# Performance work log

Hardware: AMD Instinct MI355X
Metric: run time of the kernel (lower is better)

The kernel has to match this reference:

```python
import jax, jax.numpy as jnp
import numpy as np
from jax import lax

B, C_IN, H, W = 16, 256, 64, 64
C_OUT, K_SZ, N_EXP, RED_C = 256, 3, 4, 16  # reduction_channels = max(256//16,16)=16


def setup_inputs() -> dict:
    key = jax.random.key(0)
    ks = jax.random.split(key, 6)
    x = jax.random.normal(ks[0], (B, C_IN, H, W), dtype=jnp.float32)
    # routing network params (1x1 convs == dense on pooled features)
    w1 = jax.random.normal(ks[1], (RED_C, C_IN), dtype=jnp.float32) * (1.0 / np.sqrt(C_IN))
    b1 = jnp.zeros((RED_C,), dtype=jnp.float32)
    w2 = jax.random.normal(ks[2], (N_EXP * C_IN, RED_C), dtype=jnp.float32) * (1.0 / np.sqrt(RED_C))
    b2 = jnp.zeros((N_EXP * C_IN,), dtype=jnp.float32)
    # expert weight bank (num_experts, c_out, c_in, kh, kw)
    fan_in = C_IN * K_SZ * K_SZ
    bound = np.sqrt(6.0 / fan_in)  # kaiming_uniform with a=sqrt(5) ~ U(-sqrt(6/fan_in)*..., simplified scale)
    weight = jax.random.uniform(ks[3], (N_EXP, C_OUT, C_IN, K_SZ, K_SZ), dtype=jnp.float32, minval=-bound, maxval=bound)
    return {"x": x, "w1": w1, "b1": b1, "w2": w2, "b2": b2, "weight": weight}


def reference(x, w1, b1, w2, b2, weight):
    b = x.shape[0]
    # route_func: global avg pool -> 1x1 conv -> relu -> 1x1 conv -> sigmoid
    pooled = jnp.mean(x, axis=(2, 3))                       # (b, c_in)
    r = jax.nn.relu(pooled @ w1.T + b1)                     # (b, red_c)
    rw = jax.nn.sigmoid(r @ w2.T + b2)                      # (b, K*c_in)
    rw = rw.reshape(b, N_EXP, C_IN)                         # (b, K, c_in)
    # per-sample combined kernel: sum over experts, routing scales input channels
    combined = jnp.einsum('bkc,kocij->bocij', rw, weight)   # (b, c_out, c_in, kh, kw)
    # per-sample conv (equivalent to groups=b trick in torch)
    def conv_one(xi, wi):
        return lax.conv_general_dilated(
            xi[None], wi, window_strides=(1, 1), padding=[(1, 1), (1, 1)],
            dimension_numbers=('NCHW', 'OIHW', 'NCHW'))[0]
    out = jax.vmap(conv_one)(x, combined)                   # (b, c_out, h, w)
    return out
```

## Files before the change

kernel.cpp:

```cpp
#include <hip/hip_runtime.h>
#include <hip/hip_bf16.h>
#include <math.h>

#define BB   16
#define CIN  256
#define HH   64
#define WW   64
#define COUT 256
#define NEXP 4
#define REDC 16
#define HW   (HH*WW)

typedef __attribute__((ext_vector_type(8))) short short8;
typedef __attribute__((ext_vector_type(16))) float f32x16;

#define AS1 __attribute__((address_space(1)))
#define AS3 __attribute__((address_space(3)))

__device__ __forceinline__ void gld_lds16(void* lds, const void* gp) {
    __builtin_amdgcn_global_load_lds((const AS1 unsigned int*)gp,
                                     (AS3 unsigned int*)lds, 16, 0, 0);
}

__global__ __launch_bounds__(256)
void transpose_pool_kernel(const float* __restrict__ x, ushort* __restrict__ xT,
                           float* __restrict__ pp) {
    int blk = blockIdx.x;
    int sq = blk & 3;
    int chunk = (blk >> 2) & 7;
    int b = blk >> 5;
    int c0 = chunk * 32;
    int s0 = sq * 1024;
    int tid = threadIdx.x;
    const float* xb = x + ((size_t)(b * CIN + c0)) * HW;

    float psum[32];
    #pragma unroll
    for (int i = 0; i < 32; ++i) psum[i] = 0.f;

    for (int it = 0; it < 4; ++it) {
        int s = s0 + it * 256 + tid;
        unsigned int pk[16];
        #pragma unroll
        for (int p = 0; p < 16; ++p) {
            float lo = xb[(size_t)(2 * p) * HW + s];
            float hi = xb[(size_t)(2 * p + 1) * HW + s];
            psum[2 * p]     += lo;
            psum[2 * p + 1] += hi;
            asm volatile("v_cvt_pk_bf16_f32 %0, %1, %2" : "=v"(pk[p]) : "v"(lo), "v"(hi));
        }
        #pragma unroll
        for (int q = 0; q < 4; ++q) {
            ushort* dst = xT + ((size_t)(b * 32 + chunk * 4 + q) * HW + s) * 8;
            *(uint4*)dst = make_uint4(pk[q * 4], pk[q * 4 + 1], pk[q * 4 + 2], pk[q * 4 + 3]);
        }
    }

    __shared__ float red[4][32];
    int lane = tid & 63, wid = tid >> 6;
    #pragma unroll
    for (int i = 0; i < 32; ++i) {
        float v = psum[i];
        #pragma unroll
        for (int off = 32; off > 0; off >>= 1) v += __shfl_down(v, off, 64);
        if (lane == 0) red[wid][i] = v;
    }
    __syncthreads();
    if (tid < 32)
        pp[(b * 4 + sq) * 256 + c0 + tid] = red[0][tid] + red[1][tid] + red[2][tid] + red[3][tid];
}

__global__ void route_kernel(const float* __restrict__ pp,
                             const float* __restrict__ w1, const float* __restrict__ b1,
                             const float* __restrict__ w2, const float* __restrict__ b2,
                             float* __restrict__ rw) {
    __shared__ float p_s[BB][CIN];
    __shared__ float r_s[BB][REDC];
    int tid = threadIdx.x;
    for (int i = tid; i < BB * CIN; i += 256) {
        int b = i >> 8, c = i & 255;
        p_s[b][c] = (pp[(b * 4 + 0) * 256 + c] + pp[(b * 4 + 1) * 256 + c] +
                     pp[(b * 4 + 2) * 256 + c] + pp[(b * 4 + 3) * 256 + c]) * (1.0f / HW);
    }
    __syncthreads();
    {
        int b = tid >> 4, j = tid & 15;
        float acc = b1[j];
        for (int c = 0; c < CIN; ++c) acc += p_s[b][c] * w1[j * CIN + c];
        r_s[b][j] = fmaxf(acc, 0.f);
    }
    __syncthreads();
    for (int i = tid; i < BB * NEXP * CIN; i += 256) {
        int b = i >> 10, o2 = i & 1023;
        float acc = b2[o2];
        #pragma unroll
        for (int j = 0; j < REDC; ++j) acc += r_s[b][j] * w2[o2 * REDC + j];
        rw[i] = 1.f / (1.f + expf(-acc));
    }
}

__global__ __launch_bounds__(256)
void combine3_kernel(const float* __restrict__ rw,
                     const float* __restrict__ weight,
                     ushort* __restrict__ cw) {
    int blk = blockIdx.x;
    int u = blk >> 1;
    int t = (blk & 1) * 256 + threadIdx.x;
    int gg = u & 1;
    int v = u >> 1;
    int t9 = v % 9;
    int cu = v / 9;
    int chunk16 = cu & 15;
    int ot = cu >> 4;
    int o_loc = t >> 3, c8 = t & 7;
    int o = ot * 64 + o_loc;
    int c = chunk16 * 16 + gg * 8 + c8;

    __shared__ float rw_s[16][4][8];
    int tid = threadIdx.x;
    #pragma unroll
    for (int r = 0; r < 2; ++r) {
        int i = r * 256 + tid;
        if (i < 512) {
            int b = i >> 5, k = (i >> 3) & 3, cc = i & 7;
            rw_s[b][k][cc] = rw[b * 1024 + k * 256 + chunk16 * 16 + gg * 8 + cc];
        }
    }
    __syncthreads();

    float wk0 = weight[((size_t)(0 * COUT + o) * CIN + c) * 9 + t9];
    float wk1 = weight[((size_t)(1 * COUT + o) * CIN + c) * 9 + t9];
    float wk2 = weight[((size_t)(2 * COUT + o) * CIN + c) * 9 + t9];
    float wk3 = weight[((size_t)(3 * COUT + o) * CIN + c) * 9 + t9];

    size_t base = (size_t)u * 512 + t;
    #pragma unroll
    for (int b = 0; b < 16; ++b) {
        float acc = rw_s[b][0][c8] * wk0 + rw_s[b][1][c8] * wk1 +
                    rw_s[b][2][c8] * wk2 + rw_s[b][3][c8] * wk3;
        __hip_bfloat16 hv = __float2bfloat16(acc);
        cw[base + (size_t)b * 589824] = *(ushort*)&hv;
    }
}

__global__ __launch_bounds__(512, 2)
void conv_mfma(const ushort* __restrict__ xT, const ushort* __restrict__ cw,
               float* __restrict__ out, const ushort* __restrict__ zp) {
    __shared__ char LDS[2][57472];

    int blk = blockIdx.x;
    int L = (blk & 7) * 32 + (blk >> 3);
    int b  = L >> 4;
    int rt = (L >> 2) & 3;
    int ot = L & 3;
    int r0 = rt * 16, o0 = ot * 64;
    int tid = threadIdx.x;
    int lane = tid & 63, wid = tid >> 6;
    int l31 = lane & 31, h = lane >> 5;

    f32x16 acc[2][4];
    #pragma unroll
    for (int mi = 0; mi < 2; ++mi)
        #pragma unroll
        for (int f = 0; f < 4; ++f) acc[mi][f] = (f32x16)0.f;

    const char* xTb = (const char*)(xT + (size_t)b * 32 * HW * 8);
    const ushort* Ab = cw + (size_t)((b * 4 + ot) * 16) * 9216;

    const char* srcb[7];
    int dsto[7];
    int strd[7];
    #pragma unroll
    for (int i = 0; i < 7; ++i) {
        int u = wid * 7 + i;
        if (u < 18) {
            srcb[i] = (const char*)(Ab + (size_t)u * 512) + lane * 16;
            dsto[i] = u * 1024;
            strd[i] = 18432;
        } else if (u < 54) {
            int ux = u - 18;
            int r = ux >> 1, half = ux & 1;
            int grow = r0 - 1 + r;
            bool valid = (grow >= 0 && grow < 64);
            srcb[i] = valid
                ? xTb + (size_t)(half * HW + grow * 64) * 16 + lane * 16
                : (const char*)zp + lane * 16;
            dsto[i] = 18432 + (half * 1188 + r * 66 + 1) * 16;
            strd[i] = valid ? 131072 : 0;
        } else {
            srcb[i] = (const char*)zp + lane * 16;
            dsto[i] = 56448;
            strd[i] = 0;
        }
    }

    char* ldsb = &LDS[0][0];

    for (int i = tid; i < 28736; i += 512) ((unsigned int*)ldsb)[i] = 0;
    __syncthreads();

    #define STAGE(BUF, CH)                                                    \
    {                                                                         \
        _Pragma("unroll")                                                     \
        for (int i = 0; i < 7; ++i)                                           \
            gld_lds16(ldsb + (BUF) * 57472 + dsto[i],                         \
                      srcb[i] + (size_t)(CH) * strd[i]);                      \
    }

    #define LOADT(T, va0, va1, vb0, vb1, vb2, vb3)                            \
    {                                                                         \
        const int di_ = (T) / 3, dj_ = (T) - di_ * 3;                         \
        va0 = *(const short8*)&asb[(((T) * 2 + h) * 64 + 0  + l31) * 8];      \
        va1 = *(const short8*)&asb[(((T) * 2 + h) * 64 + 32 + l31) * 8];      \
        const int rr_ = wid * 2 + di_;                                        \
        vb0 = *(const short8*)&xsb[(rr_ * 66 +  0 + l31 + dj_) * 8];          \
        vb1 = *(const short8*)&xsb[(rr_ * 66 + 32 + l31 + dj_) * 8];          \
        vb2 = *(const short8*)&xsb[((rr_ + 1) * 66 +  0 + l31 + dj_) * 8];    \
        vb3 = *(const short8*)&xsb[((rr_ + 1) * 66 + 32 + l31 + dj_) * 8];    \
    }

    #define DOMM(va0, va1, vb0, vb1, vb2, vb3)                                          \
    {                                                                                   \
        acc[0][0] = __builtin_amdgcn_mfma_f32_32x32x16_bf16(va0, vb0, acc[0][0], 0,0,0);\
        acc[1][0] = __builtin_amdgcn_mfma_f32_32x32x16_bf16(va1, vb0, acc[1][0], 0,0,0);\
        acc[0][1] = __builtin_amdgcn_mfma_f32_32x32x16_bf16(va0, vb1, acc[0][1], 0,0,0);\
        acc[1][1] = __builtin_amdgcn_mfma_f32_32x32x16_bf16(va1, vb1, acc[1][1], 0,0,0);\
        acc[0][2] = __builtin_amdgcn_mfma_f32_32x32x16_bf16(va0, vb2, acc[0][2], 0,0,0);\
        acc[1][2] = __builtin_amdgcn_mfma_f32_32x32x16_bf16(va1, vb2, acc[1][2], 0,0,0);\
        acc[0][3] = __builtin_amdgcn_mfma_f32_32x32x16_bf16(va0, vb3, acc[0][3], 0,0,0);\
        acc[1][3] = __builtin_amdgcn_mfma_f32_32x32x16_bf16(va1, vb3, acc[1][3], 0,0,0);\
    }

    STAGE(0, 0)

    #pragma unroll 1
    for (int chunk = 0; chunk < 16; ++chunk) {
        int cur = chunk & 1;
        if (chunk < 15) {
            STAGE(cur ^ 1, chunk + 1)
            asm volatile("s_waitcnt vmcnt(7)" ::: "memory");
        } else {
            asm volatile("s_waitcnt vmcnt(0)" ::: "memory");
        }
        __builtin_amdgcn_s_barrier();
        __builtin_amdgcn_sched_barrier(0);

        const ushort* asb = (const ushort*)(ldsb + cur * 57472);
        const ushort* xsb = (const ushort*)(ldsb + cur * 57472 + 18432) + h * 9504;

        short8 a0A, a1A, b0A, b1A, b2A, b3A;
        short8 a0B, a1B, b0B, b1B, b2B, b3B;

        LOADT(0, a0A, a1A, b0A, b1A, b2A, b3A)
        LOADT(1, a0B, a1B, b0B, b1B, b2B, b3B)
        DOMM(a0A, a1A, b0A, b1A, b2A, b3A)
        LOADT(2, a0A, a1A, b0A, b1A, b2A, b3A)
        DOMM(a0B, a1B, b0B, b1B, b2B, b3B)
        LOADT(3, a0B, a1B, b0B, b1B, b2B, b3B)
        DOMM(a0A, a1A, b0A, b1A, b2A, b3A)
        LOADT(4, a0A, a1A, b0A, b1A, b2A, b3A)
        DOMM(a0B, a1B, b0B, b1B, b2B, b3B)
        LOADT(5, a0B, a1B, b0B, b1B, b2B, b3B)
        DOMM(a0A, a1A, b0A, b1A, b2A, b3A)
        LOADT(6, a0A, a1A, b0A, b1A, b2A, b3A)
        DOMM(a0B, a1B, b0B, b1B, b2B, b3B)
        LOADT(7, a0B, a1B, b0B, b1B, b2B, b3B)
        DOMM(a0A, a1A, b0A, b1A, b2A, b3A)
        LOADT(8, a0A, a1A, b0A, b1A, b2A, b3A)
        DOMM(a0B, a1B, b0B, b1B, b2B, b3B)
        DOMM(a0A, a1A, b0A, b1A, b2A, b3A)

        __builtin_amdgcn_sched_barrier(0);
        __builtin_amdgcn_s_barrier();
    }

    #pragma unroll
    for (int mi = 0; mi < 2; ++mi) {
        #pragma unroll
        for (int f = 0; f < 4; ++f) {
            int pos = (r0 + wid * 2 + (f >> 1)) * 64 + (f & 1) * 32 + l31;
            #pragma unroll
            for (int j = 0; j < 16; ++j) {
                int orow = (j & 3) + 8 * (j >> 2) + 4 * h;
                out[((size_t)(b * COUT + o0 + mi * 32 + orow)) * HW + pos] = acc[mi][f][j];
            }
        }
    }
    #undef STAGE
    #undef LOADT
    #undef DOMM
}

extern "C" void kernel_launch(void* const* d_in, const int* in_sizes, int n_in,
                              void* d_out, int out_size, void* d_ws, size_t ws_size,
                              hipStream_t stream) {
    const float* x      = (const float*)d_in[0];
    const float* w1     = (const float*)d_in[1];
    const float* b1     = (const float*)d_in[2];
    const float* w2     = (const float*)d_in[3];
    const float* b2     = (const float*)d_in[4];
    const float* weight = (const float*)d_in[5];
    float* out = (float*)d_out;

    float*  ws = (float*)d_ws;
    float*  pp = ws;
    float*  rw = ws + 16384;
    ushort* cw = (ushort*)(ws + 32768);
    ushort* xT = (ushort*)(ws + 32768 + 4718592);
    ushort* zp = xT + 16777216;

    hipMemsetAsync(zp, 0, 2048, stream);
    transpose_pool_kernel<<<512, 256, 0, stream>>>(x, xT, pp);
    route_kernel<<<1, 256, 0, stream>>>(pp, w1, b1, w2, b2, rw);
    combine3_kernel<<<2304, 256, 0, stream>>>(rw, weight, cw);
    conv_mfma<<<256, 512, 0, stream>>>(xT, cw, out, zp);
}
```

Baseline: 143.2 us.

## Split chunk prefetch across three phases with barriers and MFMA priority

```diff
diff --git a/kernel.cpp b/kernel.cpp
--- a/kernel.cpp
+++ b/kernel.cpp
@@ -199,10 +199,10 @@
     for (int i = tid; i < 28736; i += 512) ((unsigned int*)ldsb)[i] = 0;
     __syncthreads();
 
-    #define STAGE(BUF, CH)                                                    \
+    #define STAGE_R(BUF, CH, I0, I1)                                          \
     {                                                                         \
         _Pragma("unroll")                                                     \
-        for (int i = 0; i < 7; ++i)                                           \
+        for (int i = (I0); i < (I1); ++i)                                     \
             gld_lds16(ldsb + (BUF) * 57472 + dsto[i],                         \
                       srcb[i] + (size_t)(CH) * strd[i]);                      \
     }
@@ -231,17 +231,19 @@
         acc[1][3] = __builtin_amdgcn_mfma_f32_32x32x16_bf16(va1, vb3, acc[1][3], 0,0,0);\
     }
 
-    STAGE(0, 0)
+    STAGE_R(0, 0, 0, 7)
 
     #pragma unroll 1
     for (int chunk = 0; chunk < 16; ++chunk) {
         int cur = chunk & 1;
+        int nxt = cur ^ 1;
         if (chunk < 15) {
-            STAGE(cur ^ 1, chunk + 1)
-            asm volatile("s_waitcnt vmcnt(7)" ::: "memory");
+            STAGE_R(nxt, chunk + 1, 0, 3)
+            asm volatile("s_waitcnt vmcnt(3)" ::: "memory");
         } else {
             asm volatile("s_waitcnt vmcnt(0)" ::: "memory");
         }
+        __builtin_amdgcn_sched_barrier(0);
         __builtin_amdgcn_s_barrier();
         __builtin_amdgcn_sched_barrier(0);
 
@@ -253,23 +255,42 @@
 
         LOADT(0, a0A, a1A, b0A, b1A, b2A, b3A)
         LOADT(1, a0B, a1B, b0B, b1B, b2B, b3B)
+        if (chunk < 15) STAGE_R(nxt, chunk + 1, 3, 5)
+        __builtin_amdgcn_sched_barrier(0);
+        __builtin_amdgcn_s_barrier();
+        __builtin_amdgcn_s_setprio(1);
         DOMM(a0A, a1A, b0A, b1A, b2A, b3A)
         LOADT(2, a0A, a1A, b0A, b1A, b2A, b3A)
         DOMM(a0B, a1B, b0B, b1B, b2B, b3B)
-        LOADT(3, a0B, a1B, b0B, b1B, b2B, b3B)
-        DOMM(a0A, a1A, b0A, b1A, b2A, b3A)
-        LOADT(4, a0A, a1A, b0A, b1A, b2A, b3A)
+        DOMM(a0A, a1A, b0A, b1A, b2A, b3A)
+        __builtin_amdgcn_s_setprio(0);
+        __builtin_amdgcn_sched_barrier(0);
+        __builtin_amdgcn_s_barrier();
+
+        LOADT(3, a0A, a1A, b0A, b1A, b2A, b3A)
+        LOADT(4, a0B, a1B, b0B, b1B, b2B, b3B)
+        if (chunk < 15) STAGE_R(nxt, chunk + 1, 5, 7)
+        __builtin_amdgcn_sched_barrier(0);
+        __builtin_amdgcn_s_barrier();
+        __builtin_amdgcn_s_setprio(1);
+        DOMM(a0A, a1A, b0A, b1A, b2A, b3A)
+        LOADT(5, a0A, a1A, b0A, b1A, b2A, b3A)
         DOMM(a0B, a1B, b0B, b1B, b2B, b3B)
-        LOADT(5, a0B, a1B, b0B, b1B, b2B, b3B)
-        DOMM(a0A, a1A, b0A, b1A, b2A, b3A)
+        DOMM(a0A, a1A, b0A, b1A, b2A, b3A)
+        __builtin_amdgcn_s_setprio(0);
+        __builtin_amdgcn_sched_barrier(0);
+        __builtin_amdgcn_s_barrier();
+
         LOADT(6, a0A, a1A, b0A, b1A, b2A, b3A)
-        DOMM(a0B, a1B, b0B, b1B, b2B, b3B)
         LOADT(7, a0B, a1B, b0B, b1B, b2B, b3B)
+        __builtin_amdgcn_sched_barrier(0);
+        __builtin_amdgcn_s_barrier();
+        __builtin_amdgcn_s_setprio(1);
         DOMM(a0A, a1A, b0A, b1A, b2A, b3A)
         LOADT(8, a0A, a1A, b0A, b1A, b2A, b3A)
         DOMM(a0B, a1B, b0B, b1B, b2B, b3B)
         DOMM(a0A, a1A, b0A, b1A, b2A, b3A)
-
+        __builtin_amdgcn_s_setprio(0);
         __builtin_amdgcn_sched_barrier(0);
         __builtin_amdgcn_s_barrier();
     }
@@ -286,7 +307,7 @@
             }
         }
     }
-    #undef STAGE
+    #undef STAGE_R
     #undef LOADT
     #undef DOMM
 }
```

Measured after the change: 146.3 us. 2.1% more time.
